# Kernel tuning notes

Measured on AMD Instinct MI355X. Metric: run time of the kernel, lower is better.

## Reference

```python
import jax, jax.numpy as jnp
import numpy as np

D_MODEL = 1024
N_HEAD = 16
D_HEAD = D_MODEL // N_HEAD
BSZ, QLEN, MLEN = 2, 1024, 1024
KLEN = QLEN + MLEN


def setup_inputs() -> dict:
    key = jax.random.key(0)
    ks = jax.random.split(key, 10)
    s = 1.0 / np.sqrt(D_MODEL)
    inp = {
        "x": jax.random.normal(ks[0], (BSZ, QLEN, D_MODEL), jnp.float32),
        "mem": jax.random.normal(ks[1], (BSZ, MLEN, D_MODEL), jnp.float32),
        "pos_emb": jax.random.normal(ks[2], (KLEN, D_MODEL), jnp.float32),
        # causal mask with memory: query i may attend to key j iff j <= i + MLEN
        "attn_mask": (jnp.arange(KLEN)[None, :] > (jnp.arange(QLEN)[:, None] + MLEN))[None, None],
        "Wq": jax.random.normal(ks[3], (D_MODEL, D_MODEL), jnp.float32) * s,
        "Wk": jax.random.normal(ks[4], (D_MODEL, D_MODEL), jnp.float32) * s,
        "Wv": jax.random.normal(ks[5], (D_MODEL, D_MODEL), jnp.float32) * s,
        "Wr": jax.random.normal(ks[6], (D_MODEL, D_MODEL), jnp.float32) * s,
        "Wo": jax.random.normal(ks[7], (D_MODEL, D_MODEL), jnp.float32) * s,
        "r_w_bias": jax.random.normal(ks[8], (N_HEAD, D_HEAD), jnp.float32) * 0.02,
        "r_r_bias": jax.random.normal(ks[9], (N_HEAD, D_HEAD), jnp.float32) * 0.02,
    }
    return inp


def _rel_shift(x):
    # x: [b, n, q, k]
    b, n, q, k = x.shape
    x_padded = jnp.pad(x, ((0, 0), (0, 0), (0, 0), (1, 0)))  # zero column at front
    x_padded = x_padded.reshape(b, n, k + 1, q)
    return x_padded[:, :, 1:].reshape(b, n, q, k)


def reference(x, mem, pos_emb, attn_mask, Wq, Wk, Wv, Wr, Wo, r_w_bias, r_r_bias):
    bsz, qlen, _ = x.shape
    k_input = jnp.concatenate([mem, x], axis=1)
    klen = k_input.shape[1]
    scale = 1.0 / np.sqrt(D_HEAD)

    # projections -> [b, n, len, d]
    q = jnp.einsum('bqe,de->bqd', x, Wq).reshape(bsz, qlen, N_HEAD, D_HEAD).transpose(0, 2, 1, 3)
    k = jnp.einsum('bke,de->bkd', k_input, Wk).reshape(bsz, klen, N_HEAD, D_HEAD).transpose(0, 2, 1, 3)
    v = jnp.einsum('bke,de->bkd', k_input, Wv).reshape(bsz, klen, N_HEAD, D_HEAD).transpose(0, 2, 1, 3)
    r = jnp.einsum('ke,de->kd', pos_emb, Wr).reshape(klen, N_HEAD, D_HEAD).transpose(1, 0, 2)  # [n,k,d]

    AC = jnp.einsum('bnqd,bnkd->bnqk', q + r_w_bias[None, :, None, :], k)
    BD = jnp.einsum('bnqd,nkd->bnqk', q + r_r_bias[None, :, None, :], r)
    BD = _rel_shift(BD)

    attn_score = (AC + BD) * scale
    attn_score = jnp.where(attn_mask, -jnp.inf, attn_score)
    attn_prob = jax.nn.softmax(attn_score, axis=-1)

    attn_vec = jnp.einsum('bnqk,bnkd->bnqd', attn_prob, v)
    attn_vec = attn_vec.transpose(0, 2, 1, 3).reshape(bsz, qlen, N_HEAD * D_HEAD)
    return jnp.einsum('bqd,ed->bqe', attn_vec, Wo)
```

## Files before the change

kernel.cpp:

```cpp
#include <hip/hip_runtime.h>


#define B_SZ 2
#define QLEN 1024
#define MLEN 1024
#define KLEN 2048
#define DMODEL 1024
#define NH 16
#define DH 64
#define NSPLIT 4

typedef _Float16 f16;
typedef __attribute__((ext_vector_type(8))) _Float16 f16x8;
typedef __attribute__((ext_vector_type(4))) _Float16 f16x4;
typedef __attribute__((ext_vector_type(4))) float f32x4;

__device__ __forceinline__ f16 f2h(float v) { return (f16)v; }
__device__ __forceinline__ float h2f(f16 v) { return (float)v; }

__device__ __forceinline__ f32x4 mfma16(f16x8 a, f16x8 b, f32x4 c) {
  return __builtin_amdgcn_mfma_f32_16x16x32_f16(a, b, c, 0, 0, 0);
}

__device__ __forceinline__ void gload_lds16(const f16* g, f16* l) {
  __builtin_amdgcn_global_load_lds(
      (const __attribute__((address_space(1))) void*)g,
      (__attribute__((address_space(3))) void*)l, 16, 0, 0);
}

__device__ __forceinline__ float bperm(int srclane, float v) {
  return __int_as_float(
      __builtin_amdgcn_ds_bpermute(srclane << 2, __float_as_int(v)));
}

__global__ __launch_bounds__(256) void convert_kernel(const float* __restrict__ src,
                                                      f16* __restrict__ dst, int n4) {
  const int i = blockIdx.x * 256 + threadIdx.x;
  if (i >= n4) return;
  const float4 v = reinterpret_cast<const float4*>(src)[i];
  f16x4 o = {(f16)v.x, (f16)v.y, (f16)v.z, (f16)v.w};
  reinterpret_cast<f16x4*>(dst)[i] = o;
}

__global__ __launch_bounds__(256) void pack_weights_kernel(
    const float* __restrict__ Wq, const float* __restrict__ Wk,
    const float* __restrict__ Wv, const float* __restrict__ Wr,
    const float* __restrict__ Wo, f16* __restrict__ Wqb, f16* __restrict__ Wkb,
    f16* __restrict__ Wvb, f16* __restrict__ Wrb, f16* __restrict__ Wob) {
  const float* src;
  f16* dst;
  switch (blockIdx.y) {
    case 0: src = Wq; dst = Wqb; break;
    case 1: src = Wk; dst = Wkb; break;
    case 2: src = Wv; dst = Wvb; break;
    case 3: src = Wr; dst = Wrb; break;
    default: src = Wo; dst = Wob; break;
  }
  const int i = blockIdx.x * 256 + threadIdx.x;
  const float4 v = reinterpret_cast<const float4*>(src)[i];
  f16x4 o = {(f16)v.x, (f16)v.y, (f16)v.z, (f16)v.w};
  reinterpret_cast<f16x4*>(dst)[i] = o;
}

__global__ __launch_bounds__(256) void build_kin_kernel(const float* __restrict__ x,
                                                        const float* __restrict__ mem,
                                                        f16* __restrict__ kin,
                                                        f16* __restrict__ xb) {
  const int i = blockIdx.x * 256 + threadIdx.x;
  const int per_b = KLEN * DMODEL / 4;
  const int b = i / per_b;
  const int rem = i - b * per_b;
  const int row = rem / (DMODEL / 4);
  const int cc = (rem - row * (DMODEL / 4)) * 4;
  const float* src = (row < MLEN)
      ? mem + ((size_t)b * MLEN + row) * DMODEL + cc
      : x + ((size_t)b * QLEN + (row - MLEN)) * DMODEL + cc;
  const float4 v = *reinterpret_cast<const float4*>(src);
  f16x4 o = {(f16)v.x, (f16)v.y, (f16)v.z, (f16)v.w};
  *reinterpret_cast<f16x4*>(kin + (size_t)i * 4) = o;
  if (row >= MLEN)
    *reinterpret_cast<f16x4*>(&xb[((size_t)b * QLEN + (row - MLEN)) * DMODEL + cc]) = o;
}

template <int DUAL, int OUT_F32>
__device__ __forceinline__ void gemm_core(const f16* __restrict__ A,
                                          const f16* __restrict__ Bm,
                                          void* __restrict__ C0v,
                                          void* __restrict__ C1v,
                                          const float* __restrict__ bias0,
                                          const float* __restrict__ bias1, int bm,
                                          int bn) {
  const int tid = threadIdx.x;
  const int wave = tid >> 6, lane = tid & 63;
  const int wr = wave >> 1, wc = wave & 1;
  const int lr = lane & 15, hi = lane >> 4;

  __shared__ f16 As[128 * 64];
  __shared__ f16 Bs[128 * 64];

  f32x4 acc[4][4];
#pragma unroll
  for (int m = 0; m < 4; ++m)
#pragma unroll
    for (int n = 0; n < 4; ++n) acc[m][n] = f32x4{0.f, 0.f, 0.f, 0.f};

  for (int k0 = 0; k0 < DMODEL; k0 += 64) {
    __syncthreads();
#pragma unroll
    for (int it = 0; it < 4; ++it) {
      const int c = it * 256 + tid;
      const int row = c >> 3, c16 = c & 7;
      const int c16s = c16 ^ (row & 7);
      gload_lds16(&A[(size_t)(bm + row) * DMODEL + k0 + c16s * 8], &As[c * 8]);
      gload_lds16(&Bm[(size_t)(bn + row) * DMODEL + k0 + c16s * 8], &Bs[c * 8]);
    }
    __syncthreads();
#pragma unroll
    for (int kk = 0; kk < 2; ++kk) {
      f16x8 af[4], bf[4];
#pragma unroll
      for (int m = 0; m < 4; ++m) {
        const int row = wr * 64 + m * 16 + lr;
        const int colf = (kk * 32 + hi * 8) ^ ((row & 7) << 3);
        af[m] = *reinterpret_cast<const f16x8*>(&As[row * 64 + colf]);
      }
#pragma unroll
      for (int n = 0; n < 4; ++n) {
        const int row = wc * 64 + n * 16 + lr;
        const int colf = (kk * 32 + hi * 8) ^ ((row & 7) << 3);
        bf[n] = *reinterpret_cast<const f16x8*>(&Bs[row * 64 + colf]);
      }
#pragma unroll
      for (int m = 0; m < 4; ++m)
#pragma unroll
        for (int n = 0; n < 4; ++n) acc[m][n] = mfma16(af[m], bf[n], acc[m][n]);
    }
  }

#pragma unroll
  for (int m = 0; m < 4; ++m)
#pragma unroll
    for (int n = 0; n < 4; ++n)
#pragma unroll
      for (int r = 0; r < 4; ++r) {
        const int grow = bm + wr * 64 + m * 16 + hi * 4 + r;
        const int gcol = bn + wc * 64 + n * 16 + lr;
        const float v = acc[m][n][r];
        if constexpr (OUT_F32) {
          reinterpret_cast<float*>(C0v)[(size_t)grow * DMODEL + gcol] = v;
        } else if constexpr (DUAL) {
          reinterpret_cast<f16*>(C0v)[(size_t)grow * DMODEL + gcol] =
              f2h((v + bias0[gcol]) * 0.125f);
          reinterpret_cast<f16*>(C1v)[(size_t)grow * DMODEL + gcol] =
              f2h((v + bias1[gcol]) * 0.125f);
        } else {
          reinterpret_cast<f16*>(C0v)[(size_t)grow * DMODEL + gcol] = f2h(v);
        }
      }
}

__global__ __launch_bounds__(256) void proj_kernel(
    const f16* __restrict__ Xb, const f16* __restrict__ Kin,
    const f16* __restrict__ Pos, const f16* __restrict__ Wqb,
    const f16* __restrict__ Wkb, const f16* __restrict__ Wvb,
    const f16* __restrict__ Wrb, f16* __restrict__ Qwb, f16* __restrict__ Qrb,
    f16* __restrict__ Kbb, f16* __restrict__ Vbb, f16* __restrict__ Rbb,
    const float* __restrict__ rwb, const float* __restrict__ rrb) {
  const int y = blockIdx.y;
  const int bn = blockIdx.x * 128;
  if (y < 16) {
    gemm_core<1, 0>(Xb, Wqb, Qwb, Qrb, rwb, rrb, y * 128, bn);
  } else if (y < 48) {
    gemm_core<0, 0>(Kin, Wkb, Kbb, nullptr, nullptr, nullptr, (y - 16) * 128, bn);
  } else if (y < 80) {
    gemm_core<0, 0>(Kin, Wvb, Vbb, nullptr, nullptr, nullptr, (y - 48) * 128, bn);
  } else {
    gemm_core<0, 0>(Pos, Wrb, Rbb, nullptr, nullptr, nullptr, (y - 80) * 128, bn);
  }
}

__global__ __launch_bounds__(256) void gemm_out_kernel(const f16* __restrict__ A,
                                                       const f16* __restrict__ Bm,
                                                       float* __restrict__ C) {
  gemm_core<0, 1>(A, Bm, C, nullptr, nullptr, nullptr, blockIdx.y * 128,
                  blockIdx.x * 128);
}

__global__ __launch_bounds__(512) void attn_kernel(
    const f16* __restrict__ Qw, const f16* __restrict__ Qr,
    const f16* __restrict__ Kb, const f16* __restrict__ Vb,
    const f16* __restrict__ Rb, float* __restrict__ Opart,
    float2* __restrict__ MLp) {
  const int bid = blockIdx.x;
  const int xcd = bid & 7, rr = bid >> 3;
  const int grp = xcd * 4 + (rr >> 5);
  const int ii = rr & 31;
  const int b = grp >> 4, n = grp & 15;
  const int qi = ii >> 2, split = ii & 3;

  const int qb = qi * 128;
  const int tid = threadIdx.x;
  const int wave = tid >> 6, lane = tid & 63;
  const int lr = lane & 15, hi = lane >> 4;
  const int t0 = hi * 4;
  const int w0 = qb + wave * 16;

  const int T = (qb + 128 + MLEN) >> 6;
  const int jt_beg = (split * T) >> 2;
  const int jt_end = ((split + 1) * T) >> 2;

  __shared__ f16 Ks[64][72];
  __shared__ f16 Vs[64][72];
  __shared__ f16 Ps[8][16][72];

  f16x8 qw[2], qr[2];
  {
    const size_t qbase = ((size_t)(b * QLEN + w0 + lr)) * DMODEL + n * DH;
#pragma unroll
    for (int kk = 0; kk < 2; ++kk) {
      qw[kk] = *reinterpret_cast<const f16x8*>(&Qw[qbase + kk * 32 + hi * 8]);
      qr[kk] = *reinterpret_cast<const f16x8*>(&Qr[qbase + kk * 32 + hi * 8]);
    }
  }

  f32x4 o[4];
#pragma unroll
  for (int df = 0; df < 4; ++df) o[df] = f32x4{0.f, 0.f, 0.f, 0.f};
  float mrow[4], lrow[4];
#pragma unroll
  for (int r = 0; r < 4; ++r) { mrow[r] = -1e30f; lrow[r] = 0.f; }

  const f16* Rn = Rb + n * DH;

  const int krow = tid >> 3, kc8 = (tid & 7) << 3;
  const int vrow = tid & 63, vc8 = ((tid >> 6) & 7) << 3;
  f16x8 kreg, vreg;
  auto issue = [&](int jt) {
    const size_t kvb = ((size_t)(b * KLEN + (jt << 6))) * DMODEL + n * DH;
    kreg = *reinterpret_cast<const f16x8*>(&Kb[kvb + (size_t)krow * DMODEL + kc8]);
    vreg = *reinterpret_cast<const f16x8*>(&Vb[kvb + (size_t)vrow * DMODEL + vc8]);
  };
  auto commit = [&]() {
    *reinterpret_cast<f16x8*>(&Ks[krow][kc8]) = kreg;
#pragma unroll
    for (int e = 0; e < 8; ++e) Vs[vc8 + e][vrow] = vreg[e];
  };

  issue(jt_beg);
  commit();
  __syncthreads();

  for (int jt = jt_beg; jt < jt_end; ++jt) {
    const bool hn = (jt + 1 < jt_end);
    if (hn) issue(jt + 1);

    const int j0 = jt << 6;

    f32x4 s[4];
#pragma unroll
    for (int nf = 0; nf < 4; ++nf) s[nf] = f32x4{0.f, 0.f, 0.f, 0.f};
#pragma unroll
    for (int kk = 0; kk < 2; ++kk)
#pragma unroll
      for (int nf = 0; nf < 4; ++nf) {
        const f16x8 kf =
            *reinterpret_cast<const f16x8*>(&Ks[nf * 16 + lr][kk * 32 + hi * 8]);
        s[nf] = mfma16(qw[kk], kf, s[nf]);
      }

    const int u0 = j0 + QLEN - 16 - w0;
    f32x4 bd[5];
#pragma unroll
    for (int nt = 0; nt < 5; ++nt) bd[nt] = f32x4{0.f, 0.f, 0.f, 0.f};
#pragma unroll
    for (int nt = 0; nt < 5; ++nt) {
      const int u = u0 + nt * 16 + lr;
      const int uc = u < KLEN ? u : KLEN - 1;
#pragma unroll
      for (int kk = 0; kk < 2; ++kk) {
        const f16x8 rf = *reinterpret_cast<const f16x8*>(
            &Rn[(size_t)uc * DMODEL + kk * 32 + hi * 8]);
        bd[nt] = mfma16(qr[kk], rf, bd[nt]);
      }
    }

#pragma unroll
    for (int r = 0; r < 4; ++r) {
      const int off = 15 - t0 - r;
      const int sl = lr + off;
      const int srclane = hi * 16 + (sl & 15);
      const bool cross = sl >= 16;
      const int i = w0 + t0 + r;
#pragma unroll
      for (int nf = 0; nf < 4; ++nf) {
        const float x0 = bperm(srclane, bd[nf][r]);
        const float x1 = bperm(srclane, bd[nf + 1][r]);
        const float bv = cross ? x1 : x0;
        const int j = j0 + nf * 16 + lr;
        s[nf][r] = (j <= i + MLEN) ? (s[nf][r] + bv) : -1e30f;
      }
    }

#pragma unroll
    for (int r = 0; r < 4; ++r) {
      float tmax = fmaxf(fmaxf(s[0][r], s[1][r]), fmaxf(s[2][r], s[3][r]));
#pragma unroll
      for (int d = 1; d < 16; d <<= 1) tmax = fmaxf(tmax, __shfl_xor(tmax, d, 64));
      const float mnew = fmaxf(mrow[r], tmax);
      const float alpha = __expf(mrow[r] - mnew);
      mrow[r] = mnew;
      float tsum = 0.f;
#pragma unroll
      for (int nf = 0; nf < 4; ++nf) {
        const float p = __expf(s[nf][r] - mnew);
        s[nf][r] = p;
        tsum += p;
      }
#pragma unroll
      for (int d = 1; d < 16; d <<= 1) tsum += __shfl_xor(tsum, d, 64);
      lrow[r] = lrow[r] * alpha + tsum;
#pragma unroll
      for (int df = 0; df < 4; ++df) o[df][r] *= alpha;
    }

#pragma unroll
    for (int nf = 0; nf < 4; ++nf)
#pragma unroll
      for (int r = 0; r < 4; ++r) Ps[wave][t0 + r][nf * 16 + lr] = f2h(s[nf][r]);

#pragma unroll
    for (int kk = 0; kk < 2; ++kk) {
      const f16x8 pa =
          *reinterpret_cast<const f16x8*>(&Ps[wave][lr][kk * 32 + hi * 8]);
#pragma unroll
      for (int df = 0; df < 4; ++df) {
        const f16x8 vb =
            *reinterpret_cast<const f16x8*>(&Vs[df * 16 + lr][kk * 32 + hi * 8]);
        o[df] = mfma16(pa, vb, o[df]);
      }
    }

    __syncthreads();
    if (hn) commit();
    __syncthreads();
  }

  const size_t obase =
      (((size_t)(split * B_SZ + b) * NH + n) * QLEN + w0 + t0) * DH;
#pragma unroll
  for (int df = 0; df < 4; ++df)
#pragma unroll
    for (int r = 0; r < 4; ++r)
      Opart[obase + (size_t)r * DH + df * 16 + lr] = o[df][r];
  if (lr == 0) {
    const size_t mbase = ((size_t)(split * B_SZ + b) * NH + n) * QLEN + w0 + t0;
#pragma unroll
    for (int r = 0; r < 4; ++r) MLp[mbase + r] = float2{mrow[r], lrow[r]};
  }
}

__global__ __launch_bounds__(256) void combine_kernel(const float* __restrict__ Op,
                                                      const float2* __restrict__ ML,
                                                      f16* __restrict__ AV) {
  const int idx = blockIdx.x * 256 + threadIdx.x;
  const int d4 = idx & 15;
  const int i = (idx >> 4) & 1023;
  const int n = (idx >> 14) & 15;
  const int b = idx >> 18;
  size_t rs[NSPLIT];
  float2 ml[NSPLIT];
#pragma unroll
  for (int s = 0; s < NSPLIT; ++s) {
    rs[s] = ((size_t)((s * B_SZ + b) * NH + n)) * QLEN + i;
    ml[s] = ML[rs[s]];
  }
  float M = ml[0].x;
#pragma unroll
  for (int s = 1; s < NSPLIT; ++s) M = fmaxf(M, ml[s].x);
  float es[NSPLIT], l = 0.f;
#pragma unroll
  for (int s = 0; s < NSPLIT; ++s) {
    es[s] = __expf(ml[s].x - M);
    l += ml[s].y * es[s];
  }
  const float inv = 1.f / l;
  float4 acc = {0.f, 0.f, 0.f, 0.f};
#pragma unroll
  for (int s = 0; s < NSPLIT; ++s) {
    const float4 ov = *reinterpret_cast<const float4*>(&Op[rs[s] * DH + d4 * 4]);
    acc.x += ov.x * es[s];
    acc.y += ov.y * es[s];
    acc.z += ov.z * es[s];
    acc.w += ov.w * es[s];
  }
  f16x4 outv;
  outv[0] = f2h(acc.x * inv);
  outv[1] = f2h(acc.y * inv);
  outv[2] = f2h(acc.z * inv);
  outv[3] = f2h(acc.w * inv);
  *reinterpret_cast<f16x4*>(&AV[((size_t)(b * QLEN + i)) * DMODEL + n * DH + d4 * 4]) =
      outv;
}

extern "C" void kernel_launch(void* const* d_in, const int* in_sizes, int n_in,
                              void* d_out, int out_size, void* d_ws, size_t ws_size,
                              hipStream_t stream) {
  (void)in_sizes; (void)n_in; (void)out_size; (void)ws_size;
  const float* x   = (const float*)d_in[0];
  const float* mem = (const float*)d_in[1];
  const float* pos = (const float*)d_in[2];
  const float* Wq  = (const float*)d_in[4];
  const float* Wk  = (const float*)d_in[5];
  const float* Wv  = (const float*)d_in[6];
  const float* Wr  = (const float*)d_in[7];
  const float* Wo  = (const float*)d_in[8];
  const float* rwb = (const float*)d_in[9];
  const float* rrb = (const float*)d_in[10];
  float* out = (float*)d_out;

  char* ws = (char*)d_ws;
  size_t off = 0;
  auto alloc = [&](size_t bytes) {
    void* p = (void*)(ws + off);
    off += (bytes + 255) & ~(size_t)255;
    return p;
  };
  f16* Xb  = (f16*)alloc((size_t)B_SZ * QLEN * DMODEL * 2);
  f16* Kin = (f16*)alloc((size_t)B_SZ * KLEN * DMODEL * 2);
  f16* Pos = (f16*)alloc((size_t)KLEN * DMODEL * 2);
  f16* Wqb = (f16*)alloc((size_t)DMODEL * DMODEL * 2);
  f16* Wkb = (f16*)alloc((size_t)DMODEL * DMODEL * 2);
  f16* Wvb = (f16*)alloc((size_t)DMODEL * DMODEL * 2);
  f16* Wrb = (f16*)alloc((size_t)DMODEL * DMODEL * 2);
  f16* Wob = (f16*)alloc((size_t)DMODEL * DMODEL * 2);
  f16* Qwb = (f16*)alloc((size_t)B_SZ * QLEN * DMODEL * 2);
  f16* Qrb = (f16*)alloc((size_t)B_SZ * QLEN * DMODEL * 2);
  f16* Kbb = (f16*)alloc((size_t)B_SZ * KLEN * DMODEL * 2);
  f16* Vbb = (f16*)alloc((size_t)B_SZ * KLEN * DMODEL * 2);
  f16* Rbb = (f16*)alloc((size_t)KLEN * DMODEL * 2);
  f16* AVb = (f16*)alloc((size_t)B_SZ * QLEN * DMODEL * 2);
  float*  Opart = (float*)alloc((size_t)NSPLIT * B_SZ * NH * QLEN * DH * 4);
  float2* MLp   = (float2*)alloc((size_t)NSPLIT * B_SZ * NH * QLEN * 8);

  pack_weights_kernel<<<dim3(1024, 5), dim3(256), 0, stream>>>(
      Wq, Wk, Wv, Wr, Wo, Wqb, Wkb, Wvb, Wrb, Wob);
  convert_kernel<<<dim3(KLEN * DMODEL / 4 / 256), dim3(256), 0, stream>>>(
      pos, Pos, KLEN * DMODEL / 4);
  build_kin_kernel<<<dim3(B_SZ * KLEN * DMODEL / 4 / 256), dim3(256), 0, stream>>>(
      x, mem, Kin, Xb);

  proj_kernel<<<dim3(8, 96), dim3(256), 0, stream>>>(
      Xb, Kin, Pos, Wqb, Wkb, Wvb, Wrb, Qwb, Qrb, Kbb, Vbb, Rbb, rwb, rrb);

  attn_kernel<<<dim3(QLEN / 128 * NSPLIT * NH * B_SZ), dim3(512), 0, stream>>>(
      Qwb, Qrb, Kbb, Vbb, Rbb, Opart, MLp);

  combine_kernel<<<dim3(B_SZ * NH * QLEN * (DH / 4) / 256), dim3(256), 0, stream>>>(
      Opart, MLp, AVb);

  gemm_out_kernel<<<dim3(DMODEL / 128, B_SZ * QLEN / 128), dim3(256), 0, stream>>>(
      AVb, Wob, out);
}
```

Before: 281.6 us.

## Halve KV splits, read K directly from global, double-buffer V, store partials in fp16

Cuts the split-K factor from 4 to 2, halving the attention grid to 512 blocks and the partial outputs the combine kernel must merge. K tiles are no longer staged in LDS; each lane loads its K fragment straight from global memory, the same way R is read. V becomes a two-slot LDS buffer so the loop needs one barrier per tile instead of two. Partial outputs are stored as fp16, and the combine kernel reads 8-wide fp16 vectors. The risks are lower occupancy from fewer blocks, uncoalesced global K reads, and some precision loss in the partials.

```diff
diff --git a/kernel.cpp b/kernel.cpp
--- a/kernel.cpp
+++ b/kernel.cpp
@@ -8,7 +8,7 @@
 #define DMODEL 1024
 #define NH 16
 #define DH 64
-#define NSPLIT 4
+#define NSPLIT 2
 
 typedef _Float16 f16;
 typedef __attribute__((ext_vector_type(8))) _Float16 f16x8;
@@ -189,14 +189,14 @@
 __global__ __launch_bounds__(512) void attn_kernel(
     const f16* __restrict__ Qw, const f16* __restrict__ Qr,
     const f16* __restrict__ Kb, const f16* __restrict__ Vb,
-    const f16* __restrict__ Rb, float* __restrict__ Opart,
+    const f16* __restrict__ Rb, f16* __restrict__ Opart,
     float2* __restrict__ MLp) {
   const int bid = blockIdx.x;
   const int xcd = bid & 7, rr = bid >> 3;
-  const int grp = xcd * 4 + (rr >> 5);
-  const int ii = rr & 31;
+  const int grp = xcd * 4 + (rr >> 4);
+  const int ii = rr & 15;
   const int b = grp >> 4, n = grp & 15;
-  const int qi = ii >> 2, split = ii & 3;
+  const int qi = ii >> 1, split = ii & 1;
 
   const int qb = qi * 128;
   const int tid = threadIdx.x;
@@ -206,11 +206,10 @@
   const int w0 = qb + wave * 16;
 
   const int T = (qb + 128 + MLEN) >> 6;
-  const int jt_beg = (split * T) >> 2;
-  const int jt_end = ((split + 1) * T) >> 2;
-
-  __shared__ f16 Ks[64][72];
-  __shared__ f16 Vs[64][72];
+  const int jt_beg = split ? (T >> 1) : 0;
+  const int jt_end = split ? T : (T >> 1);
+
+  __shared__ f16 Vs[2][64][72];
   __shared__ f16 Ps[8][16][72];
 
   f16x8 qw[2], qr[2];
@@ -231,28 +230,27 @@
   for (int r = 0; r < 4; ++r) { mrow[r] = -1e30f; lrow[r] = 0.f; }
 
   const f16* Rn = Rb + n * DH;
-
-  const int krow = tid >> 3, kc8 = (tid & 7) << 3;
+  const f16* Kn = Kb + (size_t)b * KLEN * DMODEL + n * DH;
+
   const int vrow = tid & 63, vc8 = ((tid >> 6) & 7) << 3;
-  f16x8 kreg, vreg;
-  auto issue = [&](int jt) {
-    const size_t kvb = ((size_t)(b * KLEN + (jt << 6))) * DMODEL + n * DH;
-    kreg = *reinterpret_cast<const f16x8*>(&Kb[kvb + (size_t)krow * DMODEL + kc8]);
-    vreg = *reinterpret_cast<const f16x8*>(&Vb[kvb + (size_t)vrow * DMODEL + vc8]);
+  f16x8 vreg;
+  auto issueV = [&](int jt) {
+    vreg = *reinterpret_cast<const f16x8*>(
+        &Vb[((size_t)(b * KLEN + (jt << 6)) + vrow) * DMODEL + n * DH + vc8]);
   };
-  auto commit = [&]() {
-    *reinterpret_cast<f16x8*>(&Ks[krow][kc8]) = kreg;
-#pragma unroll
-    for (int e = 0; e < 8; ++e) Vs[vc8 + e][vrow] = vreg[e];
+  auto commitV = [&](int p) {
+#pragma unroll
+    for (int e = 0; e < 8; ++e) Vs[p][vc8 + e][vrow] = vreg[e];
   };
 
-  issue(jt_beg);
-  commit();
+  issueV(jt_beg);
+  commitV(0);
   __syncthreads();
+  int p = 0;
 
   for (int jt = jt_beg; jt < jt_end; ++jt) {
     const bool hn = (jt + 1 < jt_end);
-    if (hn) issue(jt + 1);
+    if (hn) issueV(jt + 1);
 
     const int j0 = jt << 6;
 
@@ -260,13 +258,15 @@
 #pragma unroll
     for (int nf = 0; nf < 4; ++nf) s[nf] = f32x4{0.f, 0.f, 0.f, 0.f};
 #pragma unroll
-    for (int kk = 0; kk < 2; ++kk)
-#pragma unroll
-      for (int nf = 0; nf < 4; ++nf) {
+    for (int nf = 0; nf < 4; ++nf) {
+      const size_t krow = (size_t)(j0 + nf * 16 + lr) * DMODEL;
+#pragma unroll
+      for (int kk = 0; kk < 2; ++kk) {
         const f16x8 kf =
-            *reinterpret_cast<const f16x8*>(&Ks[nf * 16 + lr][kk * 32 + hi * 8]);
+            *reinterpret_cast<const f16x8*>(&Kn[krow + kk * 32 + hi * 8]);
         s[nf] = mfma16(qw[kk], kf, s[nf]);
       }
+    }
 
     const int u0 = j0 + QLEN - 16 - w0;
     f32x4 bd[5];
@@ -312,9 +312,9 @@
       float tsum = 0.f;
 #pragma unroll
       for (int nf = 0; nf < 4; ++nf) {
-        const float p = __expf(s[nf][r] - mnew);
-        s[nf][r] = p;
-        tsum += p;
+        const float pv = __expf(s[nf][r] - mnew);
+        s[nf][r] = pv;
+        tsum += pv;
       }
 #pragma unroll
       for (int d = 1; d < 16; d <<= 1) tsum += __shfl_xor(tsum, d, 64);
@@ -335,14 +335,14 @@
 #pragma unroll
       for (int df = 0; df < 4; ++df) {
         const f16x8 vb =
-            *reinterpret_cast<const f16x8*>(&Vs[df * 16 + lr][kk * 32 + hi * 8]);
+            *reinterpret_cast<const f16x8*>(&Vs[p][df * 16 + lr][kk * 32 + hi * 8]);
         o[df] = mfma16(pa, vb, o[df]);
       }
     }
 
+    if (hn) commitV(p ^ 1);
     __syncthreads();
-    if (hn) commit();
-    __syncthreads();
+    p ^= 1;
   }
 
   const size_t obase =
@@ -351,7 +351,7 @@
   for (int df = 0; df < 4; ++df)
 #pragma unroll
     for (int r = 0; r < 4; ++r)
-      Opart[obase + (size_t)r * DH + df * 16 + lr] = o[df][r];
+      Opart[obase + (size_t)r * DH + df * 16 + lr] = f2h(o[df][r]);
   if (lr == 0) {
     const size_t mbase = ((size_t)(split * B_SZ + b) * NH + n) * QLEN + w0 + t0;
 #pragma unroll
@@ -359,14 +359,14 @@
   }
 }
 
-__global__ __launch_bounds__(256) void combine_kernel(const float* __restrict__ Op,
+__global__ __launch_bounds__(256) void combine_kernel(const f16* __restrict__ Op,
                                                       const float2* __restrict__ ML,
                                                       f16* __restrict__ AV) {
   const int idx = blockIdx.x * 256 + threadIdx.x;
-  const int d4 = idx & 15;
-  const int i = (idx >> 4) & 1023;
-  const int n = (idx >> 14) & 15;
-  const int b = idx >> 18;
+  const int d8 = idx & 7;
+  const int i = (idx >> 3) & 1023;
+  const int n = (idx >> 13) & 15;
+  const int b = idx >> 17;
   size_t rs[NSPLIT];
   float2 ml[NSPLIT];
 #pragma unroll
@@ -384,21 +384,17 @@
     l += ml[s].y * es[s];
   }
   const float inv = 1.f / l;
-  float4 acc = {0.f, 0.f, 0.f, 0.f};
+  float acc[8] = {0, 0, 0, 0, 0, 0, 0, 0};
 #pragma unroll
   for (int s = 0; s < NSPLIT; ++s) {
-    const float4 ov = *reinterpret_cast<const float4*>(&Op[rs[s] * DH + d4 * 4]);
-    acc.x += ov.x * es[s];
-    acc.y += ov.y * es[s];
-    acc.z += ov.z * es[s];
-    acc.w += ov.w * es[s];
-  }
-  f16x4 outv;
-  outv[0] = f2h(acc.x * inv);
-  outv[1] = f2h(acc.y * inv);
-  outv[2] = f2h(acc.z * inv);
-  outv[3] = f2h(acc.w * inv);
-  *reinterpret_cast<f16x4*>(&AV[((size_t)(b * QLEN + i)) * DMODEL + n * DH + d4 * 4]) =
+    const f16x8 ov = *reinterpret_cast<const f16x8*>(&Op[rs[s] * DH + d8 * 8]);
+#pragma unroll
+    for (int e = 0; e < 8; ++e) acc[e] += h2f(ov[e]) * es[s];
+  }
+  f16x8 outv;
+#pragma unroll
+  for (int e = 0; e < 8; ++e) outv[e] = f2h(acc[e] * inv);
+  *reinterpret_cast<f16x8*>(&AV[((size_t)(b * QLEN + i)) * DMODEL + n * DH + d8 * 8]) =
       outv;
 }
 
@@ -439,8 +435,8 @@
   f16* Vbb = (f16*)alloc((size_t)B_SZ * KLEN * DMODEL * 2);
   f16* Rbb = (f16*)alloc((size_t)KLEN * DMODEL * 2);
   f16* AVb = (f16*)alloc((size_t)B_SZ * QLEN * DMODEL * 2);
-  float*  Opart = (float*)alloc((size_t)NSPLIT * B_SZ * NH * QLEN * DH * 4);
-  float2* MLp   = (float2*)alloc((size_t)NSPLIT * B_SZ * NH * QLEN * 8);
+  f16* Opart  = (f16*)alloc((size_t)NSPLIT * B_SZ * NH * QLEN * DH * 2);
+  float2* MLp = (float2*)alloc((size_t)NSPLIT * B_SZ * NH * QLEN * 8);
 
   pack_weights_kernel<<<dim3(1024, 5), dim3(256), 0, stream>>>(
       Wq, Wk, Wv, Wr, Wo, Wqb, Wkb, Wvb, Wrb, Wob);
@@ -455,7 +451,7 @@
   attn_kernel<<<dim3(QLEN / 128 * NSPLIT * NH * B_SZ), dim3(512), 0, stream>>>(
       Qwb, Qrb, Kbb, Vbb, Rbb, Opart, MLp);
 
-  combine_kernel<<<dim3(B_SZ * NH * QLEN * (DH / 4) / 256), dim3(256), 0, stream>>>(
+  combine_kernel<<<dim3(B_SZ * NH * QLEN * (DH / 8) / 256), dim3(256), 0, stream>>>(
       Opart, MLp, AVb);
 
   gemm_out_kernel<<<dim3(DMODEL / 128, B_SZ * QLEN / 128), dim3(256), 0, stream>>>(
```

After: 359.9 us. +27.8%, slower.
